# Optimization experiments

Measured on AMD Instinct MI355X. Metric: run time of the kernel, lower is better.

Reference implementation:

```python
import jax, jax.numpy as jnp
import numpy as np
import math

B, L, D, H, FACTOR = 4, 2048, 256, 8, 5
DH = D // H

def setup_inputs() -> dict:
    key = jax.random.key(0)
    ks = jax.random.split(key, 12)
    s = 1.0 / math.sqrt(D)
    return {
        "q": jax.random.normal(ks[0], (B, L, D), jnp.float32),
        "k": jax.random.normal(ks[1], (B, L, D), jnp.float32),
        "v": jax.random.normal(ks[2], (B, L, D), jnp.float32),
        "Wq": jax.random.normal(ks[3], (D, D), jnp.float32) * s,
        "bq": jax.random.normal(ks[4], (D,), jnp.float32) * s,
        "Wk": jax.random.normal(ks[5], (D, D), jnp.float32) * s,
        "bk": jax.random.normal(ks[6], (D,), jnp.float32) * s,
        "Wv": jax.random.normal(ks[7], (D, D), jnp.float32) * s,
        "bv": jax.random.normal(ks[8], (D,), jnp.float32) * s,
        "Wc": jax.random.normal(ks[9], (D, D), jnp.float32) * s,
        "bc": jax.random.normal(ks[10], (D,), jnp.float32) * s,
        "index_sample": jax.random.randint(ks[11], (L,), 0, L),  # U_part = min(5*L*ceil(log1p(L)), L) = L
    }

def reference(q, k, v, Wq, bq, Wk, bk, Wv, bv, Wc, bc, index_sample):
    # projections (torch Linear: x @ W^T + b)
    qp = q @ Wq.T + bq
    kp = k @ Wk.T + bk
    vp = v @ Wv.T + bv
    # NOTE: original reshapes q with a raw view (no transpose), k/v via split()
    q4 = qp.reshape(B, H, L, DH)                       # faithful to q.view(B, H, L, dh)
    k4 = kp.reshape(B, L, H, DH).transpose(0, 2, 1, 3)
    v4 = vp.reshape(B, L, H, DH).transpose(0, 2, 1, 3)
    qf = q4.reshape(B * H, L, DH)
    kf = k4.reshape(B * H, L, DH)
    vf = v4.reshape(B * H, L, DH)
    # random K sampling (with replacement); U_part == L here
    K_sample = kf[:, index_sample, :]                  # [BH, L, dh]
    QK = jnp.einsum('bld,bud->blu', qf, K_sample)      # [BH, L, L]
    M = QK.max(axis=-1) - QK.sum(axis=-1) / L          # sparsity measure [BH, L]
    u = min(FACTOR * math.ceil(math.log1p(L)), L)      # = 40
    _, top_idx = jax.lax.top_k(-M, u)                  # topk(..., largest=False)
    Q_red = jnp.take_along_axis(qf, top_idx[:, :, None], axis=1)  # [BH, u, dh]
    scores = jnp.einsum('bud,bld->bul', Q_red, kf) / math.sqrt(DH)
    probs = jax.nn.softmax(scores, axis=-1)
    out = jnp.einsum('bul,bld->bud', probs, vf)        # [BH, u, dh]
    out = out.reshape(B, H, u, DH).transpose(0, 2, 1, 3).reshape(B, u, D)
    return out @ Wc.T + bc
```

## Files before the change

### kernel.cpp

```cpp
#include <hip/hip_runtime.h>
#include <math.h>

#define B_ 4
#define L_ 2048
#define D_ 256
#define H_ 8
#define DH_ 32
#define NH_ 32
#define U_ 40
#define LD_ 524288
#define NCH_ 16

typedef __attribute__((ext_vector_type(8))) short short8;
typedef __attribute__((ext_vector_type(4))) float floatx4;

static __device__ __forceinline__ unsigned long long ullmin_(unsigned long long a, unsigned long long b) {
    return a < b ? a : b;
}
static __device__ __forceinline__ unsigned short f2bf_rne(float x) {
    unsigned u = __float_as_uint(x);
    unsigned r = u + 0x7FFFu + ((u >> 16) & 1u);
    return (unsigned short)(r >> 16);
}
static __device__ __forceinline__ float bf2f(unsigned short h) {
    return __uint_as_float(((unsigned)h) << 16);
}

__global__ __launch_bounds__(256) void wsplit(const float* __restrict__ Wq,
                                              const float* __restrict__ Wk,
                                              const float* __restrict__ Wv,
                                              unsigned short* __restrict__ Whs,
                                              unsigned short* __restrict__ Wms,
                                              unsigned short* __restrict__ Wls) {
    const int g = blockIdx.x * 256 + threadIdx.x;
    const int mat = g >> 14;
    const int rem = g & 16383;
    const int col = rem >> 6;
    const int k4 = rem & 63;
    const float* W = (mat == 0) ? Wq : (mat == 1) ? Wk : Wv;
    const float4 x = *(const float4*)(W + (size_t)col * 256 + k4 * 4);
    float xs[4] = {x.x, x.y, x.z, x.w};
    unsigned short hv[4], mv[4], lv[4];
#pragma unroll
    for (int j = 0; j < 4; ++j) {
        hv[j] = f2bf_rne(xs[j]);
        const float e1 = xs[j] - bf2f(hv[j]);
        mv[j] = f2bf_rne(e1);
        const float e2 = e1 - bf2f(mv[j]);
        lv[j] = f2bf_rne(e2);
    }
    const int colblk = col >> 6, c64 = col & 63;
    const int jt = c64 >> 4, cin = c64 & 15;
    const int kt = k4 >> 3, g8 = k4 & 7;
    const int quad = g8 >> 1, half = g8 & 1;
    const size_t o = ((((size_t)mat * 4 + colblk) * 8 + kt) << 11) +
                     jt * 512 + (quad * 16 + cin) * 8 + half * 4;
    *(ushort4*)(Whs + o) = make_ushort4(hv[0], hv[1], hv[2], hv[3]);
    *(ushort4*)(Wms + o) = make_ushort4(mv[0], mv[1], mv[2], mv[3]);
    *(ushort4*)(Wls + o) = make_ushort4(lv[0], lv[1], lv[2], lv[3]);
}

__global__ __launch_bounds__(256) void gemm_proj(const float* __restrict__ q,
                                                 const float* __restrict__ k,
                                                 const float* __restrict__ v,
                                                 const unsigned short* __restrict__ Whs,
                                                 const unsigned short* __restrict__ Wms,
                                                 const unsigned short* __restrict__ Wls,
                                                 const float* __restrict__ bq,
                                                 const float* __restrict__ bk,
                                                 const float* __restrict__ bv,
                                                 float* __restrict__ qp,
                                                 float* __restrict__ kp,
                                                 float* __restrict__ vp) {
    const int mat = blockIdx.z;
    const float* X = (mat == 0) ? q : (mat == 1) ? k : v;
    const float* bias = (mat == 0) ? bq : (mat == 1) ? bk : bv;
    float* Y = (mat == 0) ? qp : (mat == 1) ? kp : vp;
    const bool vmat = (mat == 2);

    const int t = threadIdx.x;
    const int w = t >> 6, lane = t & 63;
    const int lq = lane & 15, quad = lane >> 4;
    const int rowBase = blockIdx.x * 64 + w * 16;
    const int colBase = blockIdx.y * 128;
    const int nseg = vmat ? 16 : 24;

    __shared__ unsigned short Bls[12288];

    floatx4 acc[8];
#pragma unroll
    for (int nt2 = 0; nt2 < 8; ++nt2) acc[nt2] = (floatx4){0.f, 0.f, 0.f, 0.f};

    auto gsrc = [&](int s, int kt) -> const unsigned short* {
        const int p = s >> 3, rm = s & 7, chunk = rm >> 2, jj = rm & 3;
        const unsigned short* Wp = (p == 0) ? Whs : (p == 1) ? Wms : Wls;
        return Wp + (((((size_t)mat * 4 + ((blockIdx.y << 1) | chunk)) * 8 + kt) << 11) +
                     jj * 512 + lane * 8);
    };
    const float* xrow = X + (size_t)(rowBase + lq) * 256 + quad * 8;

    auto convertA = [&](const float4& x0, const float4& x1,
                        short8& Ah, short8& Am, short8& Al) {
        float xs[8] = {x0.x, x0.y, x0.z, x0.w, x1.x, x1.y, x1.z, x1.w};
#pragma unroll
        for (int j = 0; j < 8; ++j) {
            const unsigned short h = f2bf_rne(xs[j]);
            const float e1 = xs[j] - bf2f(h);
            const unsigned short md = f2bf_rne(e1);
            Ah[j] = (short)h;
            Am[j] = (short)md;
            if (!vmat) {
                const float e2 = e1 - bf2f(md);
                Al[j] = (short)f2bf_rne(e2);
            }
        }
    };

#pragma unroll
    for (int n = 0; n < 6; ++n) {
        const int s = w + n * 4;
        if (s < nseg)
            *(short8*)&Bls[s * 512 + lane * 8] = *(const short8*)gsrc(s, 0);
    }
    short8 Ah, Am, Al;
    {
        const float4 x0 = *(const float4*)(xrow);
        const float4 x1 = *(const float4*)(xrow + 4);
        convertA(x0, x1, Ah, Am, Al);
    }
    __syncthreads();

    for (int kt = 0; kt < 8; ++kt) {
        short8 stg[6];
        float4 nx0, nx1;
        if (kt < 7) {
#pragma unroll
            for (int n = 0; n < 6; ++n) {
                const int s = w + n * 4;
                if (s < nseg) stg[n] = *(const short8*)gsrc(s, kt + 1);
            }
            nx0 = *(const float4*)(xrow + (kt + 1) * 32);
            nx1 = *(const float4*)(xrow + (kt + 1) * 32 + 4);
        }

#pragma unroll
        for (int nt2 = 0; nt2 < 8; ++nt2) {
            const int boff = ((nt2 >> 2) << 11) + ((nt2 & 3) << 9) + lane * 8;
            const short8 Bh = *(const short8*)&Bls[boff];
            const short8 Bm = *(const short8*)&Bls[4096 + boff];
            floatx4 a = acc[nt2];
            if (!vmat) {
                const short8 Bl = *(const short8*)&Bls[8192 + boff];
                a = __builtin_amdgcn_mfma_f32_16x16x32_bf16(Am, Bm, a, 0, 0, 0);
                a = __builtin_amdgcn_mfma_f32_16x16x32_bf16(Ah, Bl, a, 0, 0, 0);
                a = __builtin_amdgcn_mfma_f32_16x16x32_bf16(Al, Bh, a, 0, 0, 0);
                a = __builtin_amdgcn_mfma_f32_16x16x32_bf16(Ah, Bm, a, 0, 0, 0);
                a = __builtin_amdgcn_mfma_f32_16x16x32_bf16(Am, Bh, a, 0, 0, 0);
                a = __builtin_amdgcn_mfma_f32_16x16x32_bf16(Ah, Bh, a, 0, 0, 0);
            } else {
                a = __builtin_amdgcn_mfma_f32_16x16x32_bf16(Ah, Bm, a, 0, 0, 0);
                a = __builtin_amdgcn_mfma_f32_16x16x32_bf16(Am, Bh, a, 0, 0, 0);
                a = __builtin_amdgcn_mfma_f32_16x16x32_bf16(Ah, Bh, a, 0, 0, 0);
            }
            acc[nt2] = a;
        }

        __syncthreads();

        if (kt < 7) {
#pragma unroll
            for (int n = 0; n < 6; ++n) {
                const int s = w + n * 4;
                if (s < nseg)
                    *(short8*)&Bls[s * 512 + lane * 8] = stg[n];
            }
            convertA(nx0, nx1, Ah, Am, Al);
        }
        __syncthreads();
    }

#pragma unroll
    for (int nt2 = 0; nt2 < 8; ++nt2) {
        const int c = colBase + nt2 * 16 + lq;
        const float bv_ = bias[c];
#pragma unroll
        for (int r = 0; r < 4; ++r) {
            const int mr = rowBase + quad * 4 + r;
            Y[(size_t)mr * 256 + c] = acc[nt2][r] + bv_;
        }
    }
}

__global__ __launch_bounds__(256) void kconv_ksum(const float* __restrict__ kp,
                                                  const int* __restrict__ idx,
                                                  unsigned short* __restrict__ Khi,
                                                  unsigned short* __restrict__ Klo,
                                                  float* __restrict__ Ksum32) {
    const int blk = blockIdx.x;
    const int i = blk >> 5, uc = blk & 31;
    const int b = i >> 3, h = i & 7;
    const int t = threadIdx.x;
    const int dq = (t & 7) * 4;
    const int ur = t >> 3;

    __shared__ float part[32][36];
    float ksum[4] = {0.f, 0.f, 0.f, 0.f};

#pragma unroll
    for (int p = 0; p < 2; ++p) {
        int u = uc * 64 + p * 32 + ur;
        const float4 x = *(const float4*)(kp + (size_t)b * LD_ + (size_t)idx[u] * D_ + h * DH_ + dq);
        float xs[4] = {x.x, x.y, x.z, x.w};
        unsigned short hv[4], lv[4];
#pragma unroll
        for (int j = 0; j < 4; ++j) {
            ksum[j] += xs[j];
            hv[j] = f2bf_rne(xs[j]);
            lv[j] = f2bf_rne(xs[j] - bf2f(hv[j]));
        }
        size_t o = ((size_t)i * 2048 + u) * 32 + dq;
        *(ushort4*)(Khi + o) = make_ushort4(hv[0], hv[1], hv[2], hv[3]);
        *(ushort4*)(Klo + o) = make_ushort4(lv[0], lv[1], lv[2], lv[3]);
    }
#pragma unroll
    for (int j = 0; j < 4; ++j) part[ur][dq + j] = ksum[j];
    __syncthreads();
    if (t < 32) {
        float s = 0.f;
#pragma unroll 8
        for (int u2 = 0; u2 < 32; ++u2) s += part[u2][t];
        Ksum32[(size_t)blk * 32 + t] = s;
    }
}

__global__ __launch_bounds__(256) void mpart_mfma(const float* __restrict__ qp,
                                                  const unsigned short* __restrict__ Khi,
                                                  const unsigned short* __restrict__ Klo,
                                                  const float* __restrict__ Ksum32,
                                                  float* __restrict__ Mv,
                                                  float* __restrict__ Qmean) {
    const int blk = blockIdx.x;
    const int i = blk >> 5;
    const int lg = blk & 31;
    const int t = threadIdx.x;
    const int w = t >> 6;
    const int lane = t & 63;
    const int lq = lane & 15;
    const int quad = lane >> 4;

    __shared__ float ssum[32];
    __shared__ float red[4][64];
    if (t < 32) {
        float s = 0.f;
#pragma unroll 8
        for (int uc = 0; uc < 32; ++uc) s += Ksum32[((size_t)i * 32 + uc) * 32 + t];
        ssum[t] = s;
    }

    short8 Ah[4], Al[4];
#pragma unroll
    for (int lt = 0; lt < 4; ++lt) {
        const int l = lg * 64 + lt * 16 + lq;
        const float* qrow = qp + ((size_t)i * 2048 + l) * 32 + quad * 8;
        float4 x0 = *(const float4*)(qrow);
        float4 x1 = *(const float4*)(qrow + 4);
        float xs[8] = {x0.x, x0.y, x0.z, x0.w, x1.x, x1.y, x1.z, x1.w};
#pragma unroll
        for (int j = 0; j < 8; ++j) {
            unsigned short h = f2bf_rne(xs[j]);
            unsigned short lo = f2bf_rne(xs[j] - bf2f(h));
            Ah[lt][j] = (short)h;
            Al[lt][j] = (short)lo;
        }
    }

    floatx4 rmax[4];
#pragma unroll
    for (int lt = 0; lt < 4; ++lt)
        rmax[lt] = (floatx4){-INFINITY, -INFINITY, -INFINITY, -INFINITY};

    const size_t kfrag = ((size_t)i * 2048 + w * 512 + lq) * 32 + quad * 8;
    const unsigned short* ph = Khi + kfrag;
    const unsigned short* pl = Klo + kfrag;
#pragma unroll 2
    for (int s = 0; s < 32; ++s) {
        short8 Bh = *(const short8*)(ph + (size_t)s * 512);
        short8 Bl = *(const short8*)(pl + (size_t)s * 512);
#pragma unroll
        for (int lt = 0; lt < 4; ++lt) {
            floatx4 acc = (floatx4){0.f, 0.f, 0.f, 0.f};
            acc = __builtin_amdgcn_mfma_f32_16x16x32_bf16(Al[lt], Bh, acc, 0, 0, 0);
            acc = __builtin_amdgcn_mfma_f32_16x16x32_bf16(Ah[lt], Bl, acc, 0, 0, 0);
            acc = __builtin_amdgcn_mfma_f32_16x16x32_bf16(Ah[lt], Bh, acc, 0, 0, 0);
#pragma unroll
            for (int r = 0; r < 4; ++r) rmax[lt][r] = fmaxf(rmax[lt][r], acc[r]);
        }
    }

#pragma unroll
    for (int lt = 0; lt < 4; ++lt)
#pragma unroll
        for (int r = 0; r < 4; ++r) {
            float v = rmax[lt][r];
#pragma unroll
            for (int off = 1; off < 16; off <<= 1)
                v = fmaxf(v, __shfl_xor(v, off, 64));
            rmax[lt][r] = v;
        }
    if (lq == 0) {
#pragma unroll
        for (int lt = 0; lt < 4; ++lt)
#pragma unroll
            for (int r = 0; r < 4; ++r)
                red[w][lt * 16 + quad * 4 + r] = rmax[lt][r];
    }
    __syncthreads();
    if (t < 64) {
        const int l = lg * 64 + t;
        float m = fmaxf(fmaxf(red[0][t], red[1][t]), fmaxf(red[2][t], red[3][t]));
        const float4* q4 = (const float4*)(qp + ((size_t)i * 2048 + l) * 32);
        const float4* s4 = (const float4*)ssum;
        float qs = 0.f;
#pragma unroll
        for (int z = 0; z < 8; ++z) {
            float4 a = q4[z];
            float4 c = s4[z];
            qs = fmaf(a.x, c.x, qs);
            qs = fmaf(a.y, c.y, qs);
            qs = fmaf(a.z, c.z, qs);
            qs = fmaf(a.w, c.w, qs);
        }
        const float qm = qs * (1.0f / 2048.0f);
        Qmean[(size_t)i * 2048 + l] = qm;
        Mv[(size_t)i * 2048 + l] = m - qm;
    }
}

__global__ __launch_bounds__(256) void topk64_fast(const float* __restrict__ Mv,
                                                   int* __restrict__ candIdx) {
    const int i = blockIdx.x;
    const int t = threadIdx.x;
    const int w = t >> 6, lane = t & 63;

    __shared__ unsigned hist[256];
    __shared__ unsigned sh_prefix, sh_selBelow;
    __shared__ unsigned cnt;
    __shared__ int candLds[64];
    __shared__ unsigned long long wred[4];

    unsigned v[8];
#pragma unroll
    for (int j = 0; j < 8; ++j) {
        const unsigned u = __float_as_uint(Mv[(size_t)i * 2048 + t + 256 * j]);
        v[j] = (u & 0x80000000u) ? ~u : (u | 0x80000000u);
    }

    if (t == 0) { sh_prefix = 0u; sh_selBelow = 0u; cnt = 0u; }

    for (int level = 0; level < 4; ++level) {
        const int shift = 24 - 8 * level;
        __syncthreads();
        const unsigned prefHi = sh_prefix;
        const unsigned selB = sh_selBelow;
        const unsigned mask = (level == 0) ? 0u : (0xFFFFFFFFu << (shift + 8));
        hist[t] = 0u;
        __syncthreads();
#pragma unroll
        for (int j = 0; j < 8; ++j)
            if ((v[j] & mask) == prefHi)
                atomicAdd(&hist[(v[j] >> shift) & 255u], 1u);
        __syncthreads();
        if (t < 64) {
            const unsigned c0 = hist[t * 4 + 0], c1 = hist[t * 4 + 1];
            const unsigned c2 = hist[t * 4 + 2], c3 = hist[t * 4 + 3];
            const unsigned i0 = c0, i1 = c0 + c1, i2 = i1 + c2, i3 = i2 + c3;
            unsigned x = i3;
#pragma unroll
            for (int off = 1; off < 64; off <<= 1) {
                const unsigned y = __shfl_up(x, off, 64);
                if (t >= off) x += y;
            }
            const unsigned excl = x - i3;
            const unsigned r = 64u - selB;
            const unsigned long long ball = __ballot(x >= r);
            const int flane = __ffsll(ball) - 1;
            if (t == flane) {
                unsigned k, ce;
                if (excl + i0 >= r)      { k = 0u; ce = excl; }
                else if (excl + i1 >= r) { k = 1u; ce = excl + i0; }
                else if (excl + i2 >= r) { k = 2u; ce = excl + i1; }
                else                     { k = 3u; ce = excl + i2; }
                sh_prefix = prefHi | (((unsigned)t * 4u + k) << shift);
                sh_selBelow = selB + ce;
            }
        }
    }
    __syncthreads();
    const unsigned thr = sh_prefix;
    const unsigned selB = sh_selBelow;
    const int rem = 64 - (int)selB;

    unsigned long long keys[8];
#pragma unroll
    for (int j = 0; j < 8; ++j) {
        const int l = t + 256 * j;
        if (v[j] < thr) {
            const unsigned p = atomicAdd(&cnt, 1u);
            candLds[p] = l;
            keys[j] = ~0ULL;
        } else if (v[j] == thr) {
            keys[j] = ((unsigned long long)v[j] << 32) | (unsigned)l;
        } else {
            keys[j] = ~0ULL;
        }
    }
    __syncthreads();

    for (int it = 0; it < rem; ++it) {
        unsigned long long best = keys[0];
#pragma unroll
        for (int j = 1; j < 8; ++j) best = ullmin_(best, keys[j]);
#pragma unroll
        for (int off = 1; off < 64; off <<= 1)
            best = ullmin_(best, __shfl_xor(best, off, 64));
        if (lane == 0) wred[w] = best;
        __syncthreads();
        const unsigned long long m = ullmin_(ullmin_(wred[0], wred[1]), ullmin_(wred[2], wred[3]));
        if (t == 0) candLds[selB + it] = (int)(m & 0xffffffffu);
#pragma unroll
        for (int j = 0; j < 8; ++j)
            if (keys[j] == m) keys[j] = ~0ULL;
        __syncthreads();
    }

    if (t < 64) candIdx[i * 64 + t] = candLds[t];
}

__global__ __launch_bounds__(256) void refine_kernel(const float* __restrict__ qp,
                                                     const float* __restrict__ kp,
                                                     const int* __restrict__ idx,
                                                     const int* __restrict__ candIdx,
                                                     float* __restrict__ refPart) {
    const int blk = blockIdx.x;
    const int i = blk >> 3, c = blk & 7;
    const int b = i >> 3, h = i & 7;
    const int t = threadIdx.x;
    __shared__ float qc[64][40];
    __shared__ float Ks[128][40];

    {
        const int cand = t >> 2, dp = (t & 3) * 8;
        const int l = candIdx[i * 64 + cand];
        const float* src = qp + ((size_t)i * 2048 + l) * 32 + dp;
        *(float4*)&qc[cand][dp] = *(const float4*)(src);
        *(float4*)&qc[cand][dp + 4] = *(const float4*)(src + 4);
    }
    __syncthreads();

    const int cand = t >> 2, usub = t & 3;
    float qv[32];
#pragma unroll
    for (int z = 0; z < 8; ++z) {
        float4 a = *(const float4*)&qc[cand][z * 4];
        qv[4 * z] = a.x; qv[4 * z + 1] = a.y; qv[4 * z + 2] = a.z; qv[4 * z + 3] = a.w;
    }

    float m = -INFINITY;
    for (int s = 0; s < 2; ++s) {
        {
            const int r = t >> 1, half = t & 1;
            const int u = c * 256 + s * 128 + r;
            const float* krow = kp + (size_t)b * LD_ + (size_t)idx[u] * D_ + h * DH_ + half * 16;
#pragma unroll
            for (int z = 0; z < 4; ++z)
                *(float4*)&Ks[r][half * 16 + z * 4] = *(const float4*)(krow + z * 4);
        }
        __syncthreads();
        for (int ur = usub; ur < 128; ur += 4) {
            float a0 = 0, a1 = 0, a2 = 0, a3 = 0;
#pragma unroll
            for (int z = 0; z < 8; ++z) {
                float4 kv = *(const float4*)&Ks[ur][z * 4];
                a0 = fmaf(qv[4 * z], kv.x, a0);
                a1 = fmaf(qv[4 * z + 1], kv.y, a1);
                a2 = fmaf(qv[4 * z + 2], kv.z, a2);
                a3 = fmaf(qv[4 * z + 3], kv.w, a3);
            }
            m = fmaxf(m, (a0 + a1) + (a2 + a3));
        }
        __syncthreads();
    }
    m = fmaxf(m, __shfl_xor(m, 1, 64));
    m = fmaxf(m, __shfl_xor(m, 2, 64));
    if ((t & 3) == 0) refPart[((size_t)i * 8 + c) * 64 + cand] = m;
}

#define SCP2 136
#define VSP 36

__global__ __launch_bounds__(320) void attn_part(const float* __restrict__ qp,
                                                 const float* __restrict__ kp,
                                                 const float* __restrict__ vp,
                                                 const int* __restrict__ candIdx,
                                                 const float* __restrict__ refPart,
                                                 const float* __restrict__ Qmean,
                                                 float* __restrict__ mPart,
                                                 float* __restrict__ sPart,
                                                 float* __restrict__ oPart) {
    const int blk = blockIdx.x;
    const int i = blk >> 4, c = blk & 15;
    const int b = i >> 3, h = i & 7;
    const int t = threadIdx.x;

    __shared__ float Qs[40][32];
    __shared__ float Vs[128][VSP];
    __shared__ float sc[40][SCP2];
    __shared__ float mred[40], sred[40];
    __shared__ int topl[40];

    if (t < 64) {
        const int l = candIdx[i * 64 + t];
        float m = -INFINITY;
#pragma unroll
        for (int cc = 0; cc < 8; ++cc) m = fmaxf(m, refPart[((size_t)i * 8 + cc) * 64 + t]);
        float Mex = m - Qmean[(size_t)i * 2048 + l];
        unsigned u32 = __float_as_uint(Mex);
        u32 = (u32 & 0x80000000u) ? ~u32 : (u32 | 0x80000000u);
        unsigned long long key = ((unsigned long long)u32 << 32) | (unsigned)l;
        for (int it = 0; it < 40; ++it) {
            unsigned long long k2 = key;
#pragma unroll
            for (int off = 1; off < 64; off <<= 1) k2 = ullmin_(k2, __shfl_xor(k2, off, 64));
            if (key == k2) {
                topl[it] = l;
                key = ~0ULL;
            }
        }
    } else {
        for (int e = t - 64; e < 1024; e += 256) {
            const int r = e >> 3, qq = e & 7;
            *(float4*)&Vs[r][qq * 4] =
                *(const float4*)(vp + (size_t)b * LD_ + (size_t)(c * 128 + r) * 256 + h * 32 + qq * 4);
        }
    }
    __syncthreads();

    {
        const int r = t >> 3, qq = t & 7;
        const int lq = topl[r];
        *(float4*)&Qs[r][qq * 4] = *(const float4*)(qp + ((size_t)i * 2048 + lq) * 32 + qq * 4);
    }
    __syncthreads();

    const float scale = 0.17677669529663687f;

    if (t < 256) {
        const int r = t >> 1;
        const int j0 = (t & 1) * 20;
        const float* kr = kp + (size_t)b * LD_ + (size_t)(c * 128 + r) * 256 + h * 32;
        float kv[32];
#pragma unroll
        for (int z = 0; z < 8; ++z) {
            float4 x = *(const float4*)(kr + z * 4);
            kv[4 * z] = x.x; kv[4 * z + 1] = x.y; kv[4 * z + 2] = x.z; kv[4 * z + 3] = x.w;
        }
#pragma unroll 4
        for (int jj = 0; jj < 20; ++jj) {
            const int j = j0 + jj;
            float a0 = 0, a1 = 0, a2 = 0, a3 = 0;
#pragma unroll
            for (int z = 0; z < 8; ++z) {
                const float4 q4 = *(const float4*)&Qs[j][z * 4];
                a0 = fmaf(kv[4 * z], q4.x, a0);
                a1 = fmaf(kv[4 * z + 1], q4.y, a1);
                a2 = fmaf(kv[4 * z + 2], q4.z, a2);
                a3 = fmaf(kv[4 * z + 3], q4.w, a3);
            }
            sc[j][r] = ((a0 + a1) + (a2 + a3)) * scale;
        }
    }
    __syncthreads();

    {
        const int w = t >> 6, lane = t & 63;
#pragma unroll
        for (int rr = 0; rr < 8; ++rr) {
            const int j = w * 8 + rr;
            float x0 = sc[j][lane], x1 = sc[j][lane + 64];
            float m = fmaxf(x0, x1);
#pragma unroll
            for (int off = 1; off < 64; off <<= 1) m = fmaxf(m, __shfl_xor(m, off, 64));
            const float e0 = __expf(x0 - m), e1 = __expf(x1 - m);
            sc[j][lane] = e0; sc[j][lane + 64] = e1;
            float s = e0 + e1;
#pragma unroll
            for (int off = 1; off < 64; off <<= 1) s += __shfl_xor(s, off, 64);
            if (lane == 0) { mred[j] = m; sred[j] = s; }
        }
    }
    __syncthreads();

    {
        const int j = t >> 3, qq = t & 7;
        float4 acc = make_float4(0.f, 0.f, 0.f, 0.f);
        for (int l = 0; l < 128; ++l) {
            const float p = sc[j][l];
            const float4 v4 = *(const float4*)&Vs[l][qq * 4];
            acc.x = fmaf(p, v4.x, acc.x);
            acc.y = fmaf(p, v4.y, acc.y);
            acc.z = fmaf(p, v4.z, acc.z);
            acc.w = fmaf(p, v4.w, acc.w);
        }
        const size_t o = (size_t)(i * NCH_ + c) * 40 + j;
        *(float4*)&oPart[o * 32 + qq * 4] = acc;
        if (qq == 0) { mPart[o] = mred[j]; sPart[o] = sred[j]; }
    }
}

__global__ __launch_bounds__(256) void attn_combine(const float* __restrict__ mPart,
                                                    const float* __restrict__ sPart,
                                                    const float* __restrict__ oPart,
                                                    float* __restrict__ attnOut) {
    const int blk = blockIdx.x;
    const int b = blk / 40, j = blk - b * 40;
    const int t = threadIdx.x;
    const int h = t >> 5, d = t & 31;
    const int i = b * 8 + h;

    float mv[NCH_];
    float M = -INFINITY;
#pragma unroll
    for (int c = 0; c < NCH_; ++c) {
        mv[c] = mPart[(size_t)(i * NCH_ + c) * 40 + j];
        M = fmaxf(M, mv[c]);
    }
    float S = 0.f, O = 0.f;
#pragma unroll
    for (int c = 0; c < NCH_; ++c) {
        const float sc_ = __expf(mv[c] - M);
        const size_t o = (size_t)(i * NCH_ + c) * 40 + j;
        S = fmaf(sPart[o], sc_, S);
        O = fmaf(oPart[o * 32 + d], sc_, O);
    }
    attnOut[((size_t)b * 40 + j) * 256 + h * 32 + d] = O / S;
}

__global__ __launch_bounds__(256) void gemm_out(const float* __restrict__ X,
                                                const float* __restrict__ Wc,
                                                const float* __restrict__ bias,
                                                float* __restrict__ Y) {
    const int t = threadIdx.x;
    const int rowBase = blockIdx.x * 16;
    const int colBase = blockIdx.y * 64;
    const int col = colBase + (t & 63);
    const int rq = (t >> 6) * 4;

    __shared__ float Xs[16][256];
#pragma unroll
    for (int e = t; e < 1024; e += 256) {
        const int r = e >> 6, kq = (e & 63) * 4;
        *(float4*)&Xs[r][kq] = *(const float4*)(X + (size_t)(rowBase + r) * 256 + kq);
    }
    __syncthreads();

    const float* wr = Wc + (size_t)col * 256;
    float acc[4] = {0.f, 0.f, 0.f, 0.f};
#pragma unroll 8
    for (int k = 0; k < 256; k += 4) {
        const float4 wv = *(const float4*)(wr + k);
#pragma unroll
        for (int r = 0; r < 4; ++r) {
            acc[r] = fmaf(Xs[rq + r][k + 0], wv.x, acc[r]);
            acc[r] = fmaf(Xs[rq + r][k + 1], wv.y, acc[r]);
            acc[r] = fmaf(Xs[rq + r][k + 2], wv.z, acc[r]);
            acc[r] = fmaf(Xs[rq + r][k + 3], wv.w, acc[r]);
        }
    }

    const float bv = bias[col];
#pragma unroll
    for (int r = 0; r < 4; ++r)
        Y[(size_t)(rowBase + rq + r) * 256 + col] = acc[r] + bv;
}

extern "C" void kernel_launch(void* const* d_in, const int* in_sizes, int n_in,
                              void* d_out, int out_size, void* d_ws, size_t ws_size,
                              hipStream_t stream) {
    const float* q  = (const float*)d_in[0];
    const float* k  = (const float*)d_in[1];
    const float* v  = (const float*)d_in[2];
    const float* Wq = (const float*)d_in[3];
    const float* bq = (const float*)d_in[4];
    const float* Wk = (const float*)d_in[5];
    const float* bk = (const float*)d_in[6];
    const float* Wv = (const float*)d_in[7];
    const float* bv = (const float*)d_in[8];
    const float* Wc = (const float*)d_in[9];
    const float* bc = (const float*)d_in[10];
    const int* idx  = (const int*)d_in[11];
    float* out = (float*)d_out;

    char* w = (char*)d_ws;
    float*          qp      = (float*)(w);
    float*          kp      = (float*)(w + (8u << 20));
    float*          vp      = (float*)(w + (16u << 20));
    unsigned short* Khi     = (unsigned short*)(w + (24u << 20));
    unsigned short* Klo     = (unsigned short*)(w + (28u << 20));
    float*          Mv      = (float*)(w + (32u << 20));
    float*          Qmean   = (float*)(w + (32u << 20) + (256u << 10));
    float*          Ksum32  = (float*)(w + (32u << 20) + (512u << 10));
    int*            candIdx = (int*)  (w + (32u << 20) + (640u << 10));
    float*          refPart = (float*)(w + (32u << 20) + (656u << 10));
    float*          attnOut = (float*)(w + (32u << 20) + (720u << 10));
    unsigned short* Whs     = (unsigned short*)(w + (40u << 20));
    unsigned short* Wms     = (unsigned short*)(w + (40u << 20) + (512u << 10));
    unsigned short* Wls     = (unsigned short*)(w + (41u << 20));
    float*          mPart   = (float*)(w + (24u << 20));
    float*          sPart   = (float*)(w + (24u << 20) + (128u << 10));
    float*          oPart   = (float*)(w + (24u << 20) + (256u << 10));

    hipLaunchKernelGGL(wsplit, dim3(192), dim3(256), 0, stream, Wq, Wk, Wv, Whs, Wms, Wls);
    hipLaunchKernelGGL(gemm_proj, dim3(128, 2, 3), dim3(256), 0, stream,
                       q, k, v, Whs, Wms, Wls, bq, bk, bv, qp, kp, vp);
    hipLaunchKernelGGL(kconv_ksum, dim3(1024), dim3(256), 0, stream, kp, idx, Khi, Klo, Ksum32);
    hipLaunchKernelGGL(mpart_mfma, dim3(1024), dim3(256), 0, stream, qp, Khi, Klo, Ksum32, Mv, Qmean);
    hipLaunchKernelGGL(topk64_fast, dim3(32), dim3(256), 0, stream, Mv, candIdx);
    hipLaunchKernelGGL(refine_kernel, dim3(256), dim3(256), 0, stream, qp, kp, idx, candIdx, refPart);
    hipLaunchKernelGGL(attn_part, dim3(512), dim3(320), 0, stream,
                       qp, kp, vp, candIdx, refPart, Qmean, mPart, sPart, oPart);
    hipLaunchKernelGGL(attn_combine, dim3(160), dim3(256), 0, stream, mPart, sPart, oPart, attnOut);
    hipLaunchKernelGGL(gemm_out, dim3(10, 4), dim3(256), 0, stream, attnOut, Wc, bc, out);
}
```

Before: 210.6 us.

## Stage sampled K fragments in double-buffered LDS and widen mpart blocks

The K hi/lo bf16 buffers are now written in an MFMA-fragment-friendly layout, so 16-row chunks are contiguous per lane fragment. mpart_mfma now uses 512-thread blocks covering 256 query rows each. K chunks are streamed through double-buffered shared memory and shared by all 8 waves, instead of each wave reading its K slice from global memory for only 64 rows. This cuts redundant global and L2 traffic for K, at the cost of fewer blocks (256), per-chunk barriers and more LDS use per block.

```diff
diff --git a/kernel.cpp b/kernel.cpp
--- a/kernel.cpp
+++ b/kernel.cpp
@@ -218,7 +218,8 @@
             hv[j] = f2bf_rne(xs[j]);
             lv[j] = f2bf_rne(xs[j] - bf2f(hv[j]));
         }
-        size_t o = ((size_t)i * 2048 + u) * 32 + dq;
+        size_t o = ((size_t)i * 2048 + (size_t)(u & ~15)) * 32 +
+                   ((dq >> 3) * 16 + (u & 15)) * 8 + (dq & 4);
         *(ushort4*)(Khi + o) = make_ushort4(hv[0], hv[1], hv[2], hv[3]);
         *(ushort4*)(Klo + o) = make_ushort4(lv[0], lv[1], lv[2], lv[3]);
     }
@@ -233,23 +234,23 @@
     }
 }
 
-__global__ __launch_bounds__(256) void mpart_mfma(const float* __restrict__ qp,
+__global__ __launch_bounds__(512) void mpart_mfma(const float* __restrict__ qp,
                                                   const unsigned short* __restrict__ Khi,
                                                   const unsigned short* __restrict__ Klo,
                                                   const float* __restrict__ Ksum32,
                                                   float* __restrict__ Mv,
                                                   float* __restrict__ Qmean) {
     const int blk = blockIdx.x;
-    const int i = blk >> 5;
-    const int lg = blk & 31;
+    const int i = blk >> 3, lg = blk & 7;
     const int t = threadIdx.x;
-    const int w = t >> 6;
-    const int lane = t & 63;
-    const int lq = lane & 15;
-    const int quad = lane >> 4;
+    const int w = t >> 6, lane = t & 63;
+    const int lq = lane & 15, quad = lane >> 4;
 
     __shared__ float ssum[32];
-    __shared__ float red[4][64];
+    __shared__ float red[256];
+    __shared__ unsigned short Kh[2][4096];
+    __shared__ unsigned short Kl[2][4096];
+
     if (t < 32) {
         float s = 0.f;
 #pragma unroll 8
@@ -257,10 +258,10 @@
         ssum[t] = s;
     }
 
-    short8 Ah[4], Al[4];
-#pragma unroll
-    for (int lt = 0; lt < 4; ++lt) {
-        const int l = lg * 64 + lt * 16 + lq;
+    short8 Ah[2], Al[2];
+#pragma unroll
+    for (int lt = 0; lt < 2; ++lt) {
+        const int l = lg * 256 + w * 32 + lt * 16 + lq;
         const float* qrow = qp + ((size_t)i * 2048 + l) * 32 + quad * 8;
         float4 x0 = *(const float4*)(qrow);
         float4 x1 = *(const float4*)(qrow + 4);
@@ -274,31 +275,49 @@
         }
     }
 
-    floatx4 rmax[4];
-#pragma unroll
-    for (int lt = 0; lt < 4; ++lt)
+    floatx4 rmax[2];
+#pragma unroll
+    for (int lt = 0; lt < 2; ++lt)
         rmax[lt] = (floatx4){-INFINITY, -INFINITY, -INFINITY, -INFINITY};
 
-    const size_t kfrag = ((size_t)i * 2048 + w * 512 + lq) * 32 + quad * 8;
-    const unsigned short* ph = Khi + kfrag;
-    const unsigned short* pl = Klo + kfrag;
-#pragma unroll 2
-    for (int s = 0; s < 32; ++s) {
-        short8 Bh = *(const short8*)(ph + (size_t)s * 512);
-        short8 Bl = *(const short8*)(pl + (size_t)s * 512);
-#pragma unroll
-        for (int lt = 0; lt < 4; ++lt) {
-            floatx4 acc = (floatx4){0.f, 0.f, 0.f, 0.f};
-            acc = __builtin_amdgcn_mfma_f32_16x16x32_bf16(Al[lt], Bh, acc, 0, 0, 0);
-            acc = __builtin_amdgcn_mfma_f32_16x16x32_bf16(Ah[lt], Bl, acc, 0, 0, 0);
-            acc = __builtin_amdgcn_mfma_f32_16x16x32_bf16(Ah[lt], Bh, acc, 0, 0, 0);
-#pragma unroll
-            for (int r = 0; r < 4; ++r) rmax[lt][r] = fmaxf(rmax[lt][r], acc[r]);
-        }
-    }
-
-#pragma unroll
-    for (int lt = 0; lt < 4; ++lt)
+    const unsigned short* gh = Khi + (size_t)i * 65536;
+    const unsigned short* gl = Klo + (size_t)i * 65536;
+
+    *(short8*)&Kh[0][t * 8] = *(const short8*)(gh + t * 8);
+    *(short8*)&Kl[0][t * 8] = *(const short8*)(gl + t * 8);
+    __syncthreads();
+
+    int buf = 0;
+    for (int uc = 0; uc < 16; ++uc) {
+        short8 sh, sl;
+        if (uc < 15) {
+            sh = *(const short8*)(gh + (uc + 1) * 4096 + t * 8);
+            sl = *(const short8*)(gl + (uc + 1) * 4096 + t * 8);
+        }
+#pragma unroll
+        for (int f = 0; f < 8; ++f) {
+            const short8 Bh = *(const short8*)&Kh[buf][f * 512 + lane * 8];
+            const short8 Bl = *(const short8*)&Kl[buf][f * 512 + lane * 8];
+#pragma unroll
+            for (int lt = 0; lt < 2; ++lt) {
+                floatx4 acc = (floatx4){0.f, 0.f, 0.f, 0.f};
+                acc = __builtin_amdgcn_mfma_f32_16x16x32_bf16(Al[lt], Bh, acc, 0, 0, 0);
+                acc = __builtin_amdgcn_mfma_f32_16x16x32_bf16(Ah[lt], Bl, acc, 0, 0, 0);
+                acc = __builtin_amdgcn_mfma_f32_16x16x32_bf16(Ah[lt], Bh, acc, 0, 0, 0);
+#pragma unroll
+                for (int r = 0; r < 4; ++r) rmax[lt][r] = fmaxf(rmax[lt][r], acc[r]);
+            }
+        }
+        if (uc < 15) {
+            *(short8*)&Kh[buf ^ 1][t * 8] = sh;
+            *(short8*)&Kl[buf ^ 1][t * 8] = sl;
+        }
+        __syncthreads();
+        buf ^= 1;
+    }
+
+#pragma unroll
+    for (int lt = 0; lt < 2; ++lt)
 #pragma unroll
         for (int r = 0; r < 4; ++r) {
             float v = rmax[lt][r];
@@ -309,15 +328,16 @@
         }
     if (lq == 0) {
 #pragma unroll
-        for (int lt = 0; lt < 4; ++lt)
+        for (int lt = 0; lt < 2; ++lt)
 #pragma unroll
             for (int r = 0; r < 4; ++r)
-                red[w][lt * 16 + quad * 4 + r] = rmax[lt][r];
-    }
-    __syncthreads();
-    if (t < 64) {
-        const int l = lg * 64 + t;
-        float m = fmaxf(fmaxf(red[0][t], red[1][t]), fmaxf(red[2][t], red[3][t]));
+                red[w * 32 + lt * 16 + quad * 4 + r] = rmax[lt][r];
+    }
+    __syncthreads();
+
+    if (t < 256) {
+        const int l = lg * 256 + t;
+        float m = red[t];
         const float4* q4 = (const float4*)(qp + ((size_t)i * 2048 + l) * 32);
         const float4* s4 = (const float4*)ssum;
         float qs = 0.f;
@@ -723,7 +743,7 @@
     hipLaunchKernelGGL(gemm_proj, dim3(128, 2, 3), dim3(256), 0, stream,
                        q, k, v, Whs, Wms, Wls, bq, bk, bv, qp, kp, vp);
     hipLaunchKernelGGL(kconv_ksum, dim3(1024), dim3(256), 0, stream, kp, idx, Khi, Klo, Ksum32);
-    hipLaunchKernelGGL(mpart_mfma, dim3(1024), dim3(256), 0, stream, qp, Khi, Klo, Ksum32, Mv, Qmean);
+    hipLaunchKernelGGL(mpart_mfma, dim3(256), dim3(512), 0, stream, qp, Khi, Klo, Ksum32, Mv, Qmean);
     hipLaunchKernelGGL(topk64_fast, dim3(32), dim3(256), 0, stream, Mv, candIdx);
     hipLaunchKernelGGL(refine_kernel, dim3(256), dim3(256), 0, stream, qp, kp, idx, candIdx, refPart);
     hipLaunchKernelGGL(attn_part, dim3(512), dim3(320), 0, stream,
```

Result: no change. 210.4 us (-0.1%).
